# Optimization experiments

Measured on AMD Instinct MI355X. Metric: run time of the kernel, lower is better.

## Reference

```python
import jax, jax.numpy as jnp
import numpy as np

N, E, D_IN, D_H, G = 50000, 800000, 300, 128, 128


def gat_conv(x, src, dst, W, att_src, att_dst, bias):
    # PyG GATConv, heads=1, concat, negative_slope=0.2, self-loops already appended.
    h = x @ W                              # [N, F]
    a_s = h @ att_src                      # [N]
    a_d = h @ att_dst                      # [N]
    e = jax.nn.leaky_relu(a_s[src] + a_d[dst], 0.2)   # [E+N]
    m = jax.ops.segment_max(e, dst, num_segments=h.shape[0])
    ex = jnp.exp(e - m[dst])
    denom = jax.ops.segment_sum(ex, dst, num_segments=h.shape[0])
    alpha = ex / denom[dst]                # softmax over in-edges of each dst
    out = jax.ops.segment_sum(alpha[:, None] * h[src], dst, num_segments=h.shape[0])
    return out + bias


def setup_inputs() -> dict:
    key = jax.random.key(0)
    ks = jax.random.split(key, 12)
    x = jax.random.normal(ks[0], (N, D_IN), dtype=jnp.float32)
    edge_index = jax.random.randint(ks[1], (2, E), 0, N)
    batch = jnp.sort(jax.random.randint(ks[2], (N,), 0, G))
    pos = jax.random.randint(ks[3], (N,), 0, 2).astype(bool)
    s = 0.05
    W1 = jax.random.normal(ks[4], (D_IN, D_H), dtype=jnp.float32) * s
    as1 = jax.random.normal(ks[5], (D_H,), dtype=jnp.float32) * s
    ad1 = jax.random.normal(ks[6], (D_H,), dtype=jnp.float32) * s
    b1 = jnp.zeros((D_H,), dtype=jnp.float32)
    W2 = jax.random.normal(ks[7], (D_H, D_H), dtype=jnp.float32) * s
    as2 = jax.random.normal(ks[8], (D_H,), dtype=jnp.float32) * s
    ad2 = jax.random.normal(ks[9], (D_H,), dtype=jnp.float32) * s
    b2 = jnp.zeros((D_H,), dtype=jnp.float32)
    Wfc = jax.random.normal(ks[10], (D_H, 1), dtype=jnp.float32) * s
    bfc = jnp.zeros((1,), dtype=jnp.float32)
    return {"x": x, "edge_index": edge_index, "batch": batch, "pos": pos,
            "num_graphs": G, "W1": W1, "as1": as1, "ad1": ad1, "b1": b1,
            "W2": W2, "as2": as2, "ad2": ad2, "b2": b2, "Wfc": Wfc, "bfc": bfc}


def reference(x, edge_index, batch, pos, num_graphs, W1, as1, ad1, b1,
              W2, as2, ad2, b2, Wfc, bfc):
    n = x.shape[0]
    loop = jnp.arange(n)
    src = jnp.concatenate([edge_index[0], loop])
    dst = jnp.concatenate([edge_index[1], loop])
    h = gat_conv(x, src, dst, W1, as1, ad1, b1)
    h = jax.nn.gelu(h, approximate=False)
    # dropout is identity in eval mode
    h = gat_conv(h, src, dst, W2, as2, ad2, b2)   # [N, 128]
    # masked per-graph mean: logits[g] = mean over nodes with batch==g and pos
    w = pos.astype(h.dtype)                       # [N]
    sums = jax.ops.segment_sum(h * w[:, None], batch, num_segments=num_graphs)
    cnt = jax.ops.segment_sum(w, batch, num_segments=num_graphs)
    logits = sums / jnp.maximum(cnt, 1.0)[:, None]          # [G, 128]
    scores = (jax.nn.gelu(logits, approximate=False) @ Wfc + bfc).reshape(-1, num_graphs)
    return scores, logits
```

## Files before the change

kernel.cpp:

```cpp
#include <hip/hip_runtime.h>
#include <math.h>

#define NN 50000
#define EE 800000
#define DIN 300
#define DH 128
#define NG 128
#define RSIZE 6250

typedef __attribute__((ext_vector_type(8))) short short8;
typedef __attribute__((ext_vector_type(4))) float floatx4;

__device__ __forceinline__ float gelu_exact(float x) {
  return 0.5f * x * (1.0f + erff(x * 0.7071067811865476f));
}

__device__ __forceinline__ void split_bf16(float v, unsigned short& hi, unsigned short& lo) {
  unsigned int u = __float_as_uint(v);
  hi = (unsigned short)(u >> 16);
  float fh = __uint_as_float((unsigned int)hi << 16);
  lo = (unsigned short)(__float_as_uint(v - fh) >> 16);
}

__device__ __forceinline__ unsigned short f2bf_rne(float x) {
  unsigned int u = __float_as_uint(x);
  unsigned int r = (u + 0x7FFFu + ((u >> 16) & 1u)) >> 16;
  return (unsigned short)r;
}

__device__ __forceinline__ float bf_lo(unsigned u) { return __uint_as_float(u << 16); }
__device__ __forceinline__ float bf_hi(unsigned u) { return __uint_as_float(u & 0xFFFF0000u); }

__device__ __forceinline__ void async_ld16(void* lds, const void* g) {
  __builtin_amdgcn_global_load_lds(
      (const __attribute__((address_space(1))) unsigned int*)(unsigned long long)g,
      (__attribute__((address_space(3))) unsigned int*)(unsigned int)(unsigned long long)lds,
      16, 0, 0);
}


__global__ __launch_bounds__(256) void count_part_kernel(const int* __restrict__ ei,
                                                         int* __restrict__ deg,
                                                         int blocksPerRange) {
  const int r = blockIdx.x & 7;
  const int t = blockIdx.x >> 3;
  const int lo = r * RSIZE, hi = lo + RSIZE;
  const int total = EE + NN;
  const int step = blocksPerRange * 256;
  for (int e0 = t * 256; e0 < total; e0 += step) {
    int e = e0 + threadIdx.x;
    if (e < total) {
      int d = (e < EE) ? ei[EE + e] : (e - EE);
      if (d >= lo && d < hi) atomicAdd(&deg[d], 1);
    }
  }
}

__global__ __launch_bounds__(1024) void scan_part_kernel(const int* __restrict__ deg,
                                                         int* __restrict__ rowptr,
                                                         int* __restrict__ bsum) {
  __shared__ int wsum[16];
  const int tid = threadIdx.x;
  const int lane = tid & 63;
  const int wid = tid >> 6;
  int idx = blockIdx.x * 1024 + tid;
  int v = (idx < NN) ? deg[idx] : 0;
  int x = v;
#pragma unroll
  for (int d = 1; d < 64; d <<= 1) {
    int y = __shfl_up(x, d, 64);
    if (lane >= d) x += y;
  }
  if (lane == 63) wsum[wid] = x;
  __syncthreads();
  if (wid == 0) {
    int s = (lane < 16) ? wsum[lane] : 0;
#pragma unroll
    for (int d = 1; d < 16; d <<= 1) {
      int y = __shfl_up(s, d, 64);
      if (lane >= d) s += y;
    }
    if (lane < 16) wsum[lane] = s;
  }
  __syncthreads();
  int woff = (wid > 0) ? wsum[wid - 1] : 0;
  int incl = x + woff;
  if (idx < NN) rowptr[idx] = incl - v;
  if (tid == 1023) bsum[blockIdx.x] = incl;
}

__global__ __launch_bounds__(64) void scan_sums_kernel(const int* __restrict__ bsum,
                                                       int* __restrict__ boff, int nb) {
  int lane = threadIdx.x;
  int v = (lane < nb) ? bsum[lane] : 0;
  int x = v;
#pragma unroll
  for (int d = 1; d < 64; d <<= 1) {
    int y = __shfl_up(x, d, 64);
    if (lane >= d) x += y;
  }
  if (lane < nb) boff[lane] = x - v;
  if (lane == nb - 1) boff[nb] = x;
}

__global__ __launch_bounds__(256) void scan_add_kernel(int* __restrict__ rowptr,
                                                       const int* __restrict__ boff,
                                                       int* __restrict__ cursor, int nb) {
  int i = blockIdx.x * 256 + threadIdx.x;
  if (i < NN) {
    int r = rowptr[i] + boff[i >> 10];
    rowptr[i] = r;
    cursor[i] = r;
  } else if (i == NN) {
    rowptr[NN] = boff[nb];
  }
}

__global__ __launch_bounds__(256) void scatter_part_kernel(const int* __restrict__ ei,
                                                           int* __restrict__ cursor,
                                                           int* __restrict__ colA,
                                                           int blocksPerRange) {
  const int r = blockIdx.x & 7;
  const int t = blockIdx.x >> 3;
  const int lo = r * RSIZE, hi = lo + RSIZE;
  const int total = EE + NN;
  const int step = blocksPerRange * 256;
  for (int e0 = t * 256; e0 < total; e0 += step) {
    int e = e0 + threadIdx.x;
    if (e < total) {
      int d = (e < EE) ? ei[EE + e] : (e - EE);
      if (d >= lo && d < hi) {
        int s = (e < EE) ? ei[e] : d;
        int p = atomicAdd(&cursor[d], 1);
        colA[p] = s;
      }
    }
  }
}


__global__ __launch_bounds__(256) void convert_bt_kernel(const float* __restrict__ B,
                                                         unsigned short* __restrict__ Bth,
                                                         unsigned short* __restrict__ Btl,
                                                         int K, int Kpad) {
  int i = blockIdx.x * 256 + threadIdx.x;
  int n = i / Kpad, k = i % Kpad;
  if (n >= 128) return;
  float v = (k < K) ? B[(long)k * 128 + n] : 0.f;
  unsigned short h, l;
  split_bf16(v, h, l);
  Bth[(long)n * Kpad + k] = h;
  Btl[(long)n * Kpad + k] = l;
}


__global__ __launch_bounds__(256) void gemm_mfma_kernel(
    const float* __restrict__ A,
    const unsigned short* __restrict__ Bth, const unsigned short* __restrict__ Btl,
    unsigned short* __restrict__ C, int M, int K, int Kpad,
    const float* __restrict__ avs, const float* __restrict__ avd,
    float* __restrict__ aS, float* __restrict__ aD) {
  __shared__ __align__(16) unsigned short Bls[2][2][128 * 32];

  const int tid = threadIdx.x;
  const int lane = tid & 63;
  const int w = tid >> 6;
  const int q = lane >> 4;
  const int m16 = lane & 15;
  const int row0 = blockIdx.x * 64;
  const int myrow = row0 + w * 16 + m16;
  const bool rok = myrow < M;
  const long abase = (long)myrow * K;

  const int rl = lane >> 2, qq0 = lane & 3;
  const int nb0 = w * 16 + rl;
  const int nb1 = 64 + w * 16 + rl;
  const long boff0 = (long)nb0 * Kpad + (long)((qq0 ^ ((nb0 >> 1) & 3)) * 8);
  const long boff1 = (long)nb1 * Kpad + (long)((qq0 ^ ((nb1 >> 1) & 3)) * 8);

  floatx4 acc[8];
#pragma unroll
  for (int i = 0; i < 8; i++) acc[i] = (floatx4)(0.f);

  const int nsteps = Kpad / 32;

  float4 vA0, vA1, nA0, nA1;
  nA0 = nA1 = make_float4(0.f, 0.f, 0.f, 0.f);

  auto stageB = [&](int s, int nb) {
    const int k0 = s * 32;
    async_ld16(&Bls[nb][0][(w * 16) * 32], Bth + boff0 + k0);
    async_ld16(&Bls[nb][0][(64 + w * 16) * 32], Bth + boff1 + k0);
    async_ld16(&Bls[nb][1][(w * 16) * 32], Btl + boff0 + k0);
    async_ld16(&Bls[nb][1][(64 + w * 16) * 32], Btl + boff1 + k0);
  };
  auto loadA = [&](int s, float4& x0, float4& x1) {
    const int k0 = s * 32 + q * 8;
    x0 = make_float4(0.f, 0.f, 0.f, 0.f);
    x1 = x0;
    if (rok) {
      if (k0 + 4 <= K) x0 = *(const float4*)&A[abase + k0];
      if (k0 + 8 <= K) x1 = *(const float4*)&A[abase + k0 + 4];
    }
  };

  stageB(0, 0);
  loadA(0, vA0, vA1);
  __syncthreads();

  for (int s = 0; s < nsteps; s++) {
    const int cur = s & 1;
    if (s + 1 < nsteps) {
      stageB(s + 1, 1 ^ cur);
      loadA(s + 1, nA0, nA1);
    }
    float av[8] = {vA0.x, vA0.y, vA0.z, vA0.w, vA1.x, vA1.y, vA1.z, vA1.w};
    union {
      unsigned u[4];
      short8 s8;
    } Uh, Ul;
#pragma unroll
    for (int i = 0; i < 4; i++) {
      unsigned short ha, la, hb, lb;
      split_bf16(av[2 * i], ha, la);
      split_bf16(av[2 * i + 1], hb, lb);
      Uh.u[i] = (unsigned)ha | ((unsigned)hb << 16);
      Ul.u[i] = (unsigned)la | ((unsigned)lb << 16);
    }
    short8 afh = Uh.s8, afl = Ul.s8;
#pragma unroll
    for (int ct = 0; ct < 8; ct++) {
      int n = ct * 16 + m16;
      int qv = (q ^ ((n >> 1) & 3)) * 8;
      short8 bfh = *(const short8*)&Bls[cur][0][n * 32 + qv];
      short8 bfl = *(const short8*)&Bls[cur][1][n * 32 + qv];
      acc[ct] = __builtin_amdgcn_mfma_f32_16x16x32_bf16(afh, bfh, acc[ct], 0, 0, 0);
      acc[ct] = __builtin_amdgcn_mfma_f32_16x16x32_bf16(afh, bfl, acc[ct], 0, 0, 0);
      acc[ct] = __builtin_amdgcn_mfma_f32_16x16x32_bf16(afl, bfh, acc[ct], 0, 0, 0);
    }
    vA0 = nA0;
    vA1 = nA1;
    __syncthreads();
  }

  float avs_r[8], avd_r[8];
#pragma unroll
  for (int ct = 0; ct < 8; ct++) {
    avs_r[ct] = avs[ct * 16 + m16];
    avd_r[ct] = avd[ct * 16 + m16];
  }
#pragma unroll
  for (int reg = 0; reg < 4; reg++) {
    int grow = row0 + w * 16 + q * 4 + reg;
    bool ok = grow < M;
    float ps = 0.f, pd = 0.f;
#pragma unroll
    for (int ct = 0; ct < 8; ct++) {
      float c = acc[ct][reg];
      if (ok) C[(long)grow * 128 + ct * 16 + m16] = f2bf_rne(c);
      ps = fmaf(c, avs_r[ct], ps);
      pd = fmaf(c, avd_r[ct], pd);
    }
#pragma unroll
    for (int d = 1; d < 16; d <<= 1) {
      ps += __shfl_xor(ps, d, 64);
      pd += __shfl_xor(pd, d, 64);
    }
    if (m16 == 0 && ok) {
      aS[grow] = ps;
      aD[grow] = pd;
    }
  }
}


__global__ __launch_bounds__(256) void aggregate_kernel(const int* __restrict__ rowptr,
                                                        const int* __restrict__ colA,
                                                        const float* __restrict__ aS,
                                                        const float* __restrict__ aD,
                                                        const unsigned short* __restrict__ Hb,
                                                        const float* __restrict__ bias,
                                                        float* __restrict__ out,
                                                        int apply_gelu) {
  const int lane = threadIdx.x & 63;
  const int dst = blockIdx.x * 4 + (threadIdx.x >> 6);
  if (dst >= NN) return;
  const int start = rowptr[dst];
  const int end = rowptr[dst + 1];
  const int deg = end - start;
  const float ad = aD[dst];
  const int half = lane >> 5;
  const int fl = lane & 31;

  float a0 = 0.f, a1 = 0.f, a2 = 0.f, a3 = 0.f;

  if (deg <= 64) {
    int src = 0;
    float e = -__builtin_inff();
    if (lane < deg) {
      src = colA[start + lane];
      float v = aS[src] + ad;
      e = (v > 0.f) ? v : 0.2f * v;
    }
    float mx = e;
#pragma unroll
    for (int d = 1; d < 64; d <<= 1) mx = fmaxf(mx, __shfl_xor(mx, d, 64));
    float ew = (lane < deg) ? expf(e - mx) : 0.f;
    float ss = ew;
#pragma unroll
    for (int d = 1; d < 64; d <<= 1) ss += __shfl_xor(ss, d, 64);
    float wgt = ew * (1.f / ss);
    for (int j = 0; j < deg; j += 4) {
      int j0 = j + half;
      int j1 = j + 2 + half;
      int sj0 = __shfl(src, j0, 64);
      float wj0 = __shfl(wgt, j0, 64);
      int sj1 = __shfl(src, j1, 64);
      float wj1 = __shfl(wgt, j1, 64);
      uint2 u0 = *(const uint2*)&Hb[(long)sj0 * DH + fl * 4];
      uint2 u1 = *(const uint2*)&Hb[(long)sj1 * DH + fl * 4];
      a0 = fmaf(wj0, bf_lo(u0.x), a0);
      a1 = fmaf(wj0, bf_hi(u0.x), a1);
      a2 = fmaf(wj0, bf_lo(u0.y), a2);
      a3 = fmaf(wj0, bf_hi(u0.y), a3);
      a0 = fmaf(wj1, bf_lo(u1.x), a0);
      a1 = fmaf(wj1, bf_hi(u1.x), a1);
      a2 = fmaf(wj1, bf_lo(u1.y), a2);
      a3 = fmaf(wj1, bf_hi(u1.y), a3);
    }
  } else {
    float m = -__builtin_inff(), ssum = 0.f;
    for (int c0 = start; c0 < end; c0 += 64) {
      int i = c0 + lane;
      float e = -__builtin_inff();
      if (i < end) {
        int s = colA[i];
        float v = aS[s] + ad;
        e = (v > 0.f) ? v : 0.2f * v;
      }
      float cm = e;
#pragma unroll
      for (int d = 1; d < 64; d <<= 1) cm = fmaxf(cm, __shfl_xor(cm, d, 64));
      float ce = (i < end) ? expf(e - cm) : 0.f;
      float cs = ce;
#pragma unroll
      for (int d = 1; d < 64; d <<= 1) cs += __shfl_xor(cs, d, 64);
      float nm = fmaxf(m, cm);
      ssum = ssum * expf(m - nm) + cs * expf(cm - nm);
      m = nm;
    }
    float inv = 1.f / ssum;
    for (int c0 = start; c0 < end; c0 += 64) {
      int i = c0 + lane;
      int src = 0;
      float wgt = 0.f;
      if (i < end) {
        src = colA[i];
        float v = aS[src] + ad;
        float e = (v > 0.f) ? v : 0.2f * v;
        wgt = expf(e - m) * inv;
      }
      int lim = min(64, end - c0);
      for (int j = 0; j < lim; j += 4) {
        int j0 = j + half;
        int j1 = j + 2 + half;
        int sj0 = __shfl(src, j0, 64);
        float wj0 = __shfl(wgt, j0, 64);
        int sj1 = __shfl(src, j1, 64);
        float wj1 = __shfl(wgt, j1, 64);
        uint2 u0 = *(const uint2*)&Hb[(long)sj0 * DH + fl * 4];
        uint2 u1 = *(const uint2*)&Hb[(long)sj1 * DH + fl * 4];
        a0 = fmaf(wj0, bf_lo(u0.x), a0);
        a1 = fmaf(wj0, bf_hi(u0.x), a1);
        a2 = fmaf(wj0, bf_lo(u0.y), a2);
        a3 = fmaf(wj0, bf_hi(u0.y), a3);
        a0 = fmaf(wj1, bf_lo(u1.x), a0);
        a1 = fmaf(wj1, bf_hi(u1.x), a1);
        a2 = fmaf(wj1, bf_lo(u1.y), a2);
        a3 = fmaf(wj1, bf_hi(u1.y), a3);
      }
    }
  }

  a0 += __shfl_xor(a0, 32, 64);
  a1 += __shfl_xor(a1, 32, 64);
  a2 += __shfl_xor(a2, 32, 64);
  a3 += __shfl_xor(a3, 32, 64);

  if (half == 0) {
    float4 b = *(const float4*)&bias[fl * 4];
    float r0 = a0 + b.x;
    float r1 = a1 + b.y;
    float r2 = a2 + b.z;
    float r3 = a3 + b.w;
    if (apply_gelu) {
      r0 = gelu_exact(r0); r1 = gelu_exact(r1);
      r2 = gelu_exact(r2); r3 = gelu_exact(r3);
    }
    *(float4*)&out[(long)dst * DH + fl * 4] = make_float4(r0, r1, r2, r3);
  }
}


__global__ __launch_bounds__(128) void pool_kernel(const float* __restrict__ H,
                                                   const int* __restrict__ batch,
                                                   const int* __restrict__ pos,
                                                   float* __restrict__ sums,
                                                   float* __restrict__ cnt) {
  const int CH = 64;
  int n0 = blockIdx.x * CH;
  int n1 = min(n0 + CH, NN);
  int f = threadIdx.x;
  float acc = 0.f, c = 0.f;
  int g = batch[n0];
  for (int n = n0; n < n1; n++) {
    int gn = batch[n];
    if (gn != g) {
      atomicAdd(&sums[g * DH + f], acc);
      if (f == 0) atomicAdd(&cnt[g], c);
      acc = 0.f; c = 0.f; g = gn;
    }
    if (pos[n]) {
      acc += H[(long)n * DH + f];
      c += 1.f;
    }
  }
  atomicAdd(&sums[g * DH + f], acc);
  if (f == 0) atomicAdd(&cnt[g], c);
}


__global__ __launch_bounds__(128) void head_kernel(const float* __restrict__ sums,
                                                   const float* __restrict__ cnt,
                                                   const float* __restrict__ Wfc,
                                                   const float* __restrict__ bfc,
                                                   float* __restrict__ out) {
  int g = blockIdx.x;
  int f = threadIdx.x;
  float c = fmaxf(cnt[g], 1.f);
  float logit = sums[g * DH + f] / c;
  out[NG + g * DH + f] = logit;
  float gl = gelu_exact(logit) * Wfc[f];
  __shared__ float red[2];
#pragma unroll
  for (int d = 1; d < 64; d <<= 1) gl += __shfl_xor(gl, d, 64);
  int lane = f & 63, w = f >> 6;
  if (lane == 0) red[w] = gl;
  __syncthreads();
  if (f == 0) out[g] = red[0] + red[1] + bfc[0];
}


extern "C" void kernel_launch(void* const* d_in, const int* in_sizes, int n_in,
                              void* d_out, int out_size, void* d_ws, size_t ws_size,
                              hipStream_t stream) {
  const float* x   = (const float*)d_in[0];
  const int* ei    = (const int*)d_in[1];
  const int* batch = (const int*)d_in[2];
  const int* pos   = (const int*)d_in[3];
  const float* W1  = (const float*)d_in[5];
  const float* as1 = (const float*)d_in[6];
  const float* ad1 = (const float*)d_in[7];
  const float* b1  = (const float*)d_in[8];
  const float* W2  = (const float*)d_in[9];
  const float* as2 = (const float*)d_in[10];
  const float* ad2 = (const float*)d_in[11];
  const float* b2  = (const float*)d_in[12];
  const float* Wfc = (const float*)d_in[13];
  const float* bfc = (const float*)d_in[14];
  float* out = (float*)d_out;

  const int KP1 = 320;
  const int KP2 = 128;
  const int NB_SCAN = (NN + 1023) / 1024;
  const int BPR = 416;

  char* ws = (char*)d_ws;
  size_t off = 0;
  auto nxt = [&](size_t b) -> void* {
    size_t p = off;
    off += (b + 255) & ~(size_t)255;
    return (void*)(ws + p);
  };
  int* rowptr = (int*)nxt((NN + 1) * sizeof(int));
  int* cursor = (int*)nxt(NN * sizeof(int));
  int* colA   = (int*)nxt((size_t)(EE + NN) * sizeof(int));
  int* bsum   = (int*)nxt((NB_SCAN + 1) * sizeof(int));
  int* boff   = (int*)nxt((NB_SCAN + 1) * sizeof(int));
  float* aS   = (float*)nxt((size_t)2 * NN * sizeof(float));
  float* aD   = aS + NN;
  unsigned short* bufAb = (unsigned short*)nxt((size_t)NN * DH * sizeof(short));
  float* bufB = (float*)nxt((size_t)NN * DH * sizeof(float));
  float* sums = (float*)nxt((size_t)(NG * DH + NG) * sizeof(float));
  float* cnt  = sums + NG * DH;
  unsigned short* Bt1h = (unsigned short*)nxt((size_t)128 * KP1 * sizeof(short));
  unsigned short* Bt1l = (unsigned short*)nxt((size_t)128 * KP1 * sizeof(short));
  unsigned short* Bt2h = (unsigned short*)nxt((size_t)128 * KP2 * sizeof(short));
  unsigned short* Bt2l = (unsigned short*)nxt((size_t)128 * KP2 * sizeof(short));

  hipMemsetAsync(cursor, 0, NN * sizeof(int), stream);
  hipMemsetAsync(sums, 0, (NG * DH + NG) * sizeof(float), stream);

  convert_bt_kernel<<<(128 * KP1 + 255) / 256, 256, 0, stream>>>(W1, Bt1h, Bt1l, DIN, KP1);
  convert_bt_kernel<<<(128 * KP2 + 255) / 256, 256, 0, stream>>>(W2, Bt2h, Bt2l, DH, KP2);

  count_part_kernel<<<8 * BPR, 256, 0, stream>>>(ei, cursor, BPR);
  scan_part_kernel<<<NB_SCAN, 1024, 0, stream>>>(cursor, rowptr, bsum);
  scan_sums_kernel<<<1, 64, 0, stream>>>(bsum, boff, NB_SCAN);
  scan_add_kernel<<<(NN + 1 + 255) / 256, 256, 0, stream>>>(rowptr, boff, cursor, NB_SCAN);
  scatter_part_kernel<<<8 * BPR, 256, 0, stream>>>(ei, cursor, colA, BPR);

  const int gblocks = (NN + 63) / 64;
  gemm_mfma_kernel<<<gblocks, 256, 0, stream>>>(x, Bt1h, Bt1l, bufAb, NN, DIN, KP1,
                                                as1, ad1, aS, aD);
  aggregate_kernel<<<(NN + 3) / 4, 256, 0, stream>>>(rowptr, colA, aS, aD, bufAb, b1, bufB, 1);
  gemm_mfma_kernel<<<gblocks, 256, 0, stream>>>(bufB, Bt2h, Bt2l, bufAb, NN, DH, KP2,
                                                as2, ad2, aS, aD);
  aggregate_kernel<<<(NN + 3) / 4, 256, 0, stream>>>(rowptr, colA, aS, aD, bufAb, b2, bufB, 0);
  pool_kernel<<<(NN + 63) / 64, 128, 0, stream>>>(bufB, batch, pos, sums, cnt);
  head_kernel<<<NG, 128, 0, stream>>>(sums, cnt, Wfc, bfc, out);
}
```

Measured before the change: 344.4 us.

## Split GEMM tile across waves by columns and deepen aggregate gather unrolling

The GEMM block now covers 32 rows instead of 64, with its four waves arranged 2x2 (two row groups by two column halves). This doubles the grid and halves per-wave accumulators, and the attention dot products are combined across the column halves through shared memory with an extra barrier. The low-degree aggregate path now issues four gathered row loads per iteration instead of two, zeroing weights for out-of-range edges and masking shuffle indices. The aim is more occupancy and memory-level parallelism, at the cost of loading each B tile for half as many rows and some wasted loads on tail edges.

```diff
diff --git a/kernel.cpp b/kernel.cpp
--- a/kernel.cpp
+++ b/kernel.cpp
@@ -165,10 +165,12 @@
   const int tid = threadIdx.x;
   const int lane = tid & 63;
   const int w = tid >> 6;
+  const int wr = w & 1;
+  const int wc = w >> 1;
   const int q = lane >> 4;
   const int m16 = lane & 15;
-  const int row0 = blockIdx.x * 64;
-  const int myrow = row0 + w * 16 + m16;
+  const int row0 = blockIdx.x * 32;
+  const int myrow = row0 + wr * 16 + m16;
   const bool rok = myrow < M;
   const long abase = (long)myrow * K;
 
@@ -178,9 +180,9 @@
   const long boff0 = (long)nb0 * Kpad + (long)((qq0 ^ ((nb0 >> 1) & 3)) * 8);
   const long boff1 = (long)nb1 * Kpad + (long)((qq0 ^ ((nb1 >> 1) & 3)) * 8);
 
-  floatx4 acc[8];
-#pragma unroll
-  for (int i = 0; i < 8; i++) acc[i] = (floatx4)(0.f);
+  floatx4 acc[4];
+#pragma unroll
+  for (int i = 0; i < 4; i++) acc[i] = (floatx4)(0.f);
 
   const int nsteps = Kpad / 32;
 
@@ -229,8 +231,8 @@
     }
     short8 afh = Uh.s8, afl = Ul.s8;
 #pragma unroll
-    for (int ct = 0; ct < 8; ct++) {
-      int n = ct * 16 + m16;
+    for (int ct = 0; ct < 4; ct++) {
+      int n = wc * 64 + ct * 16 + m16;
       int qv = (q ^ ((n >> 1) & 3)) * 8;
       short8 bfh = *(const short8*)&Bls[cur][0][n * 32 + qv];
       short8 bfl = *(const short8*)&Bls[cur][1][n * 32 + qv];
@@ -243,21 +245,22 @@
     __syncthreads();
   }
 
-  float avs_r[8], avd_r[8];
-#pragma unroll
-  for (int ct = 0; ct < 8; ct++) {
-    avs_r[ct] = avs[ct * 16 + m16];
-    avd_r[ct] = avd[ct * 16 + m16];
-  }
+  float avs_r[4], avd_r[4];
+#pragma unroll
+  for (int ct = 0; ct < 4; ct++) {
+    avs_r[ct] = avs[wc * 64 + ct * 16 + m16];
+    avd_r[ct] = avd[wc * 64 + ct * 16 + m16];
+  }
+  float psA[4], pdA[4];
 #pragma unroll
   for (int reg = 0; reg < 4; reg++) {
-    int grow = row0 + w * 16 + q * 4 + reg;
+    int grow = row0 + wr * 16 + q * 4 + reg;
     bool ok = grow < M;
     float ps = 0.f, pd = 0.f;
 #pragma unroll
-    for (int ct = 0; ct < 8; ct++) {
+    for (int ct = 0; ct < 4; ct++) {
       float c = acc[ct][reg];
-      if (ok) C[(long)grow * 128 + ct * 16 + m16] = f2bf_rne(c);
+      if (ok) C[(long)grow * 128 + wc * 64 + ct * 16 + m16] = f2bf_rne(c);
       ps = fmaf(c, avs_r[ct], ps);
       pd = fmaf(c, avd_r[ct], pd);
     }
@@ -266,9 +269,29 @@
       ps += __shfl_xor(ps, d, 64);
       pd += __shfl_xor(pd, d, 64);
     }
-    if (m16 == 0 && ok) {
-      aS[grow] = ps;
-      aD[grow] = pd;
+    psA[reg] = ps;
+    pdA[reg] = pd;
+  }
+  float* redS = (float*)&Bls[0][0][0];
+  float* redD = redS + 32;
+  if (wc == 1 && m16 == 0) {
+#pragma unroll
+    for (int reg = 0; reg < 4; reg++) {
+      int rloc = wr * 16 + q * 4 + reg;
+      redS[rloc] = psA[reg];
+      redD[rloc] = pdA[reg];
+    }
+  }
+  __syncthreads();
+  if (wc == 0 && m16 == 0) {
+#pragma unroll
+    for (int reg = 0; reg < 4; reg++) {
+      int rloc = wr * 16 + q * 4 + reg;
+      int grow = row0 + rloc;
+      if (grow < M) {
+        aS[grow] = psA[reg] + redS[rloc];
+        aD[grow] = pdA[reg] + redD[rloc];
+      }
     }
   }
 }
@@ -310,23 +333,26 @@
 #pragma unroll
     for (int d = 1; d < 64; d <<= 1) ss += __shfl_xor(ss, d, 64);
     float wgt = ew * (1.f / ss);
-    for (int j = 0; j < deg; j += 4) {
-      int j0 = j + half;
-      int j1 = j + 2 + half;
-      int sj0 = __shfl(src, j0, 64);
-      float wj0 = __shfl(wgt, j0, 64);
-      int sj1 = __shfl(src, j1, 64);
-      float wj1 = __shfl(wgt, j1, 64);
-      uint2 u0 = *(const uint2*)&Hb[(long)sj0 * DH + fl * 4];
-      uint2 u1 = *(const uint2*)&Hb[(long)sj1 * DH + fl * 4];
-      a0 = fmaf(wj0, bf_lo(u0.x), a0);
-      a1 = fmaf(wj0, bf_hi(u0.x), a1);
-      a2 = fmaf(wj0, bf_lo(u0.y), a2);
-      a3 = fmaf(wj0, bf_hi(u0.y), a3);
-      a0 = fmaf(wj1, bf_lo(u1.x), a0);
-      a1 = fmaf(wj1, bf_hi(u1.x), a1);
-      a2 = fmaf(wj1, bf_lo(u1.y), a2);
-      a3 = fmaf(wj1, bf_hi(u1.y), a3);
+    for (int j = 0; j < deg; j += 8) {
+      int sj[4];
+      float wj[4];
+#pragma unroll
+      for (int i = 0; i < 4; i++) {
+        int idx = j + 2 * i + half;
+        sj[i] = __shfl(src, idx & 63, 64);
+        float ww = __shfl(wgt, idx & 63, 64);
+        wj[i] = (idx < deg) ? ww : 0.f;
+      }
+      uint2 u[4];
+#pragma unroll
+      for (int i = 0; i < 4; i++) u[i] = *(const uint2*)&Hb[(long)sj[i] * DH + fl * 4];
+#pragma unroll
+      for (int i = 0; i < 4; i++) {
+        a0 = fmaf(wj[i], bf_lo(u[i].x), a0);
+        a1 = fmaf(wj[i], bf_hi(u[i].x), a1);
+        a2 = fmaf(wj[i], bf_lo(u[i].y), a2);
+        a3 = fmaf(wj[i], bf_hi(u[i].y), a3);
+      }
     }
   } else {
     float m = -__builtin_inff(), ssum = 0.f;
@@ -364,10 +390,12 @@
       for (int j = 0; j < lim; j += 4) {
         int j0 = j + half;
         int j1 = j + 2 + half;
-        int sj0 = __shfl(src, j0, 64);
-        float wj0 = __shfl(wgt, j0, 64);
-        int sj1 = __shfl(src, j1, 64);
-        float wj1 = __shfl(wgt, j1, 64);
+        int sj0 = __shfl(src, j0 & 63, 64);
+        float wj0 = __shfl(wgt, j0 & 63, 64);
+        if (j0 >= lim) wj0 = 0.f;
+        int sj1 = __shfl(src, j1 & 63, 64);
+        float wj1 = __shfl(wgt, j1 & 63, 64);
+        if (j1 >= lim) wj1 = 0.f;
         uint2 u0 = *(const uint2*)&Hb[(long)sj0 * DH + fl * 4];
         uint2 u1 = *(const uint2*)&Hb[(long)sj1 * DH + fl * 4];
         a0 = fmaf(wj0, bf_lo(u0.x), a0);
@@ -510,7 +538,7 @@
   scan_add_kernel<<<(NN + 1 + 255) / 256, 256, 0, stream>>>(rowptr, boff, cursor, NB_SCAN);
   scatter_part_kernel<<<8 * BPR, 256, 0, stream>>>(ei, cursor, colA, BPR);
 
-  const int gblocks = (NN + 63) / 64;
+  const int gblocks = (NN + 31) / 32;
   gemm_mfma_kernel<<<gblocks, 256, 0, stream>>>(x, Bt1h, Bt1l, bufAb, NN, DIN, KP1,
                                                 as1, ad1, aS, aD);
   aggregate_kernel<<<(NN + 3) / 4, 256, 0, stream>>>(rowptr, colA, aS, aD, bufAb, b1, bufB, 1);
```

Measured after the change: 348.4 us. Within noise of the previous version (+1.2%).

## Load GEMM B fragments directly to registers; widen gather unroll in aggregation

Applied to the files above, without the earlier changes.

The GEMM stops staging the split-bf16 weight tiles through double-buffered LDS with async global-to-LDS loads and barriers. Each wave now reads its B fragments straight from global memory (L2-cached) into registers every k-step, which removes the LDS traffic and the __syncthreads calls but re-reads the same weights from every wave. The aggregation loop for small-degree nodes is unrolled to four gathered rows per iteration, with weights masked to zero past the degree, to keep more loads in flight. The large-degree path adds matching bounds masking on its shuffled indices.

```diff
diff --git a/kernel.cpp b/kernel.cpp
--- a/kernel.cpp
+++ b/kernel.cpp
@@ -30,13 +30,6 @@
 
 __device__ __forceinline__ float bf_lo(unsigned u) { return __uint_as_float(u << 16); }
 __device__ __forceinline__ float bf_hi(unsigned u) { return __uint_as_float(u & 0xFFFF0000u); }
-
-__device__ __forceinline__ void async_ld16(void* lds, const void* g) {
-  __builtin_amdgcn_global_load_lds(
-      (const __attribute__((address_space(1))) unsigned int*)(unsigned long long)g,
-      (__attribute__((address_space(3))) unsigned int*)(unsigned int)(unsigned long long)lds,
-      16, 0, 0);
-}
 
 
 __global__ __launch_bounds__(256) void count_part_kernel(const int* __restrict__ ei,
@@ -160,23 +153,15 @@
     unsigned short* __restrict__ C, int M, int K, int Kpad,
     const float* __restrict__ avs, const float* __restrict__ avd,
     float* __restrict__ aS, float* __restrict__ aD) {
-  __shared__ __align__(16) unsigned short Bls[2][2][128 * 32];
-
-  const int tid = threadIdx.x;
-  const int lane = tid & 63;
-  const int w = tid >> 6;
+  const int lane = threadIdx.x & 63;
+  const int w = threadIdx.x >> 6;
   const int q = lane >> 4;
   const int m16 = lane & 15;
-  const int row0 = blockIdx.x * 64;
-  const int myrow = row0 + w * 16 + m16;
+  const int row0 = blockIdx.x * 64 + w * 16;
+  const int myrow = row0 + m16;
   const bool rok = myrow < M;
   const long abase = (long)myrow * K;
-
-  const int rl = lane >> 2, qq0 = lane & 3;
-  const int nb0 = w * 16 + rl;
-  const int nb1 = 64 + w * 16 + rl;
-  const long boff0 = (long)nb0 * Kpad + (long)((qq0 ^ ((nb0 >> 1) & 3)) * 8);
-  const long boff1 = (long)nb1 * Kpad + (long)((qq0 ^ ((nb1 >> 1) & 3)) * 8);
+  const long bbase = (long)m16 * Kpad + q * 8;
 
   floatx4 acc[8];
 #pragma unroll
@@ -185,15 +170,6 @@
   const int nsteps = Kpad / 32;
 
   float4 vA0, vA1, nA0, nA1;
-  nA0 = nA1 = make_float4(0.f, 0.f, 0.f, 0.f);
-
-  auto stageB = [&](int s, int nb) {
-    const int k0 = s * 32;
-    async_ld16(&Bls[nb][0][(w * 16) * 32], Bth + boff0 + k0);
-    async_ld16(&Bls[nb][0][(64 + w * 16) * 32], Bth + boff1 + k0);
-    async_ld16(&Bls[nb][1][(w * 16) * 32], Btl + boff0 + k0);
-    async_ld16(&Bls[nb][1][(64 + w * 16) * 32], Btl + boff1 + k0);
-  };
   auto loadA = [&](int s, float4& x0, float4& x1) {
     const int k0 = s * 32 + q * 8;
     x0 = make_float4(0.f, 0.f, 0.f, 0.f);
@@ -204,16 +180,17 @@
     }
   };
 
-  stageB(0, 0);
   loadA(0, vA0, vA1);
-  __syncthreads();
 
   for (int s = 0; s < nsteps; s++) {
-    const int cur = s & 1;
-    if (s + 1 < nsteps) {
-      stageB(s + 1, 1 ^ cur);
-      loadA(s + 1, nA0, nA1);
-    }
+    short8 bfh[8], bfl[8];
+    const long bofs = bbase + s * 32;
+#pragma unroll
+    for (int ct = 0; ct < 8; ct++) {
+      bfh[ct] = *(const short8*)&Bth[bofs + (long)ct * 16 * Kpad];
+      bfl[ct] = *(const short8*)&Btl[bofs + (long)ct * 16 * Kpad];
+    }
+    if (s + 1 < nsteps) loadA(s + 1, nA0, nA1);
     float av[8] = {vA0.x, vA0.y, vA0.z, vA0.w, vA1.x, vA1.y, vA1.z, vA1.w};
     union {
       unsigned u[4];
@@ -230,17 +207,12 @@
     short8 afh = Uh.s8, afl = Ul.s8;
 #pragma unroll
     for (int ct = 0; ct < 8; ct++) {
-      int n = ct * 16 + m16;
-      int qv = (q ^ ((n >> 1) & 3)) * 8;
-      short8 bfh = *(const short8*)&Bls[cur][0][n * 32 + qv];
-      short8 bfl = *(const short8*)&Bls[cur][1][n * 32 + qv];
-      acc[ct] = __builtin_amdgcn_mfma_f32_16x16x32_bf16(afh, bfh, acc[ct], 0, 0, 0);
-      acc[ct] = __builtin_amdgcn_mfma_f32_16x16x32_bf16(afh, bfl, acc[ct], 0, 0, 0);
-      acc[ct] = __builtin_amdgcn_mfma_f32_16x16x32_bf16(afl, bfh, acc[ct], 0, 0, 0);
+      acc[ct] = __builtin_amdgcn_mfma_f32_16x16x32_bf16(afh, bfh[ct], acc[ct], 0, 0, 0);
+      acc[ct] = __builtin_amdgcn_mfma_f32_16x16x32_bf16(afh, bfl[ct], acc[ct], 0, 0, 0);
+      acc[ct] = __builtin_amdgcn_mfma_f32_16x16x32_bf16(afl, bfh[ct], acc[ct], 0, 0, 0);
     }
     vA0 = nA0;
     vA1 = nA1;
-    __syncthreads();
   }
 
   float avs_r[8], avd_r[8];
@@ -251,7 +223,7 @@
   }
 #pragma unroll
   for (int reg = 0; reg < 4; reg++) {
-    int grow = row0 + w * 16 + q * 4 + reg;
+    int grow = row0 + q * 4 + reg;
     bool ok = grow < M;
     float ps = 0.f, pd = 0.f;
 #pragma unroll
@@ -310,23 +282,26 @@
 #pragma unroll
     for (int d = 1; d < 64; d <<= 1) ss += __shfl_xor(ss, d, 64);
     float wgt = ew * (1.f / ss);
-    for (int j = 0; j < deg; j += 4) {
-      int j0 = j + half;
-      int j1 = j + 2 + half;
-      int sj0 = __shfl(src, j0, 64);
-      float wj0 = __shfl(wgt, j0, 64);
-      int sj1 = __shfl(src, j1, 64);
-      float wj1 = __shfl(wgt, j1, 64);
-      uint2 u0 = *(const uint2*)&Hb[(long)sj0 * DH + fl * 4];
-      uint2 u1 = *(const uint2*)&Hb[(long)sj1 * DH + fl * 4];
-      a0 = fmaf(wj0, bf_lo(u0.x), a0);
-      a1 = fmaf(wj0, bf_hi(u0.x), a1);
-      a2 = fmaf(wj0, bf_lo(u0.y), a2);
-      a3 = fmaf(wj0, bf_hi(u0.y), a3);
-      a0 = fmaf(wj1, bf_lo(u1.x), a0);
-      a1 = fmaf(wj1, bf_hi(u1.x), a1);
-      a2 = fmaf(wj1, bf_lo(u1.y), a2);
-      a3 = fmaf(wj1, bf_hi(u1.y), a3);
+    for (int j = 0; j < deg; j += 8) {
+      int sj[4];
+      float wj[4];
+#pragma unroll
+      for (int i = 0; i < 4; i++) {
+        int idx = j + 2 * i + half;
+        sj[i] = __shfl(src, idx & 63, 64);
+        float ww = __shfl(wgt, idx & 63, 64);
+        wj[i] = (idx < deg) ? ww : 0.f;
+      }
+      uint2 u[4];
+#pragma unroll
+      for (int i = 0; i < 4; i++) u[i] = *(const uint2*)&Hb[(long)sj[i] * DH + fl * 4];
+#pragma unroll
+      for (int i = 0; i < 4; i++) {
+        a0 = fmaf(wj[i], bf_lo(u[i].x), a0);
+        a1 = fmaf(wj[i], bf_hi(u[i].x), a1);
+        a2 = fmaf(wj[i], bf_lo(u[i].y), a2);
+        a3 = fmaf(wj[i], bf_hi(u[i].y), a3);
+      }
     }
   } else {
     float m = -__builtin_inff(), ssum = 0.f;
@@ -364,10 +339,12 @@
       for (int j = 0; j < lim; j += 4) {
         int j0 = j + half;
         int j1 = j + 2 + half;
-        int sj0 = __shfl(src, j0, 64);
-        float wj0 = __shfl(wgt, j0, 64);
-        int sj1 = __shfl(src, j1, 64);
-        float wj1 = __shfl(wgt, j1, 64);
+        int sj0 = __shfl(src, j0 & 63, 64);
+        float wj0 = __shfl(wgt, j0 & 63, 64);
+        if (j0 >= lim) wj0 = 0.f;
+        int sj1 = __shfl(src, j1 & 63, 64);
+        float wj1 = __shfl(wgt, j1 & 63, 64);
+        if (j1 >= lim) wj1 = 0.f;
         uint2 u0 = *(const uint2*)&Hb[(long)sj0 * DH + fl * 4];
         uint2 u1 = *(const uint2*)&Hb[(long)sj1 * DH + fl * 4];
         a0 = fmaf(wj0, bf_lo(u0.x), a0);
```

Measured after the change: 407.9 us. +18.5%, slower.
